# Kernel optimization log

Measured on AMD Instinct MI355X. Metric: run time of the kernel, lower is better.

The kernel has to match this reference:

```python
import jax, jax.numpy as jnp
import numpy as np

EPS = 1e-6
LOSS_WEIGHT = 1.0


def setup_inputs() -> dict:
    key = jax.random.key(0)
    k1, k2 = jax.random.split(key)
    pred = jax.random.normal(k1, (32, 2048, 2), dtype=jnp.float32)
    target = jax.random.normal(k2, (32, 2048, 2), dtype=jnp.float32)
    return {"pred": pred, "target": target}


def reference(pred, target):
    # Pairwise distances: [B, N1, N2]
    diff = pred[:, :, None, :] - target[:, None, :, :]
    sq = jnp.sum(diff * diff, axis=-1)
    dist = jnp.sqrt(sq + EPS)
    # Bidirectional Chamfer per batch item: [B]
    forward_chamfer = jnp.mean(jnp.min(dist, axis=2), axis=1)
    backward_chamfer = jnp.mean(jnp.min(dist, axis=1), axis=1)
    chamfer = forward_chamfer + backward_chamfer
    # reduction='mean' over batch -> scalar, scaled by loss_weight
    return LOSS_WEIGHT * jnp.mean(chamfer)
```

## Files before the change

kernel.cpp:

```cpp
#include <hip/hip_runtime.h>
#include <math.h>
#include <float.h>

#define B 32
#define N 2048
#define EPS 1e-6f
#define TILE 256
#define CHUNK 512
#define NCHUNK (N / CHUNK)
#define NTILES (N / TILE)
#define NQ_TOTAL (2 * B * N)

__global__ __launch_bounds__(256) void chamfer_min_kernel(
    const float* __restrict__ pred, const float* __restrict__ target,
    float* __restrict__ pmin) {
  const int tile = blockIdx.x;
  const int c    = blockIdx.y;
  const int db   = blockIdx.z;
  const int dir  = db >> 5;
  const int b    = db & 31;

  const float* qbase = (dir == 0) ? pred : target;
  const float* rbase = (dir == 0) ? target : pred;

  __shared__ float4 L[3 * CHUNK / 4];

  {
    const float4* rsrc = (const float4*)(rbase + (size_t)b * N * 2);
    float4 rv = rsrc[c * (CHUNK / 2) + threadIdx.x];
    float rx2a = -2.f * rv.x, ry2a = -2.f * rv.y;
    float rx2b = -2.f * rv.z, ry2b = -2.f * rv.w;
    float cra  = fmaf(rv.x, rv.x, rv.y * rv.y);
    float crb  = fmaf(rv.z, rv.z, rv.w * rv.w);
    float* Lf = (float*)L;
    const int base = 12 * (threadIdx.x >> 1) + 2 * (threadIdx.x & 1);
    *(float2*)(Lf + base + 0) = make_float2(rx2a, rx2b);
    *(float2*)(Lf + base + 4) = make_float2(ry2a, ry2b);
    *(float2*)(Lf + base + 8) = make_float2(cra,  crb);
  }
  __syncthreads();

  const int qi = tile * TILE + threadIdx.x;
  const float2 q = ((const float2*)(qbase + (size_t)b * N * 2))[qi];

  float m0 = FLT_MAX, m1 = FLT_MAX;
#pragma unroll 4
  for (int jj = 0; jj < CHUNK / 4; ++jj) {
    float4 X = L[3 * jj];
    float4 Y = L[3 * jj + 1];
    float4 C = L[3 * jj + 2];
    float d0 = fmaf(X.x, q.x, fmaf(Y.x, q.y, C.x));
    float d1 = fmaf(X.y, q.x, fmaf(Y.y, q.y, C.y));
    float d2 = fmaf(X.z, q.x, fmaf(Y.z, q.y, C.z));
    float d3 = fmaf(X.w, q.x, fmaf(Y.w, q.y, C.w));
    m0 = fminf(fminf(m0, d0), d1);
    m1 = fminf(fminf(m1, d2), d3);
  }
  const float qq = fmaf(q.x, q.x, q.y * q.y);
  pmin[((size_t)db * NCHUNK + c) * N + qi] = fminf(m0, m1) + qq;
}

__global__ __launch_bounds__(256) void chamfer_combine_kernel(
    const float* __restrict__ pmin, float* __restrict__ partial2) {
  const int g  = blockIdx.x * 256 + threadIdx.x;
  const int db = g >> 11;
  const int qi = g & 2047;
  const float* p = pmin + (size_t)db * NCHUNK * N + qi;
  float v = fminf(fminf(p[0], p[N]), fminf(p[2 * N], p[3 * N]));
  float s = sqrtf(fmaxf(v, 0.f) + EPS);
#pragma unroll
  for (int off = 32; off > 0; off >>= 1)
    s += __shfl_down(s, off, 64);
  __shared__ float wsum[4];
  const int wid = threadIdx.x >> 6;
  if ((threadIdx.x & 63) == 0) wsum[wid] = s;
  __syncthreads();
  if (threadIdx.x == 0)
    partial2[blockIdx.x] = wsum[0] + wsum[1] + wsum[2] + wsum[3];
}

__global__ __launch_bounds__(512) void chamfer_final_kernel(
    const float* __restrict__ partial2, float* __restrict__ out) {
  float v = partial2[threadIdx.x];
#pragma unroll
  for (int off = 32; off > 0; off >>= 1)
    v += __shfl_down(v, off, 64);
  __shared__ float wsum[8];
  if ((threadIdx.x & 63) == 0) wsum[threadIdx.x >> 6] = v;
  __syncthreads();
  if (threadIdx.x == 0) {
    float s = 0.f;
#pragma unroll
    for (int i = 0; i < 8; ++i) s += wsum[i];
    out[0] = s * (1.0f / (float)(B * N));
  }
}

extern "C" void kernel_launch(void* const* d_in, const int* in_sizes, int n_in,
                              void* d_out, int out_size, void* d_ws, size_t ws_size,
                              hipStream_t stream) {
  const float* pred   = (const float*)d_in[0];
  const float* target = (const float*)d_in[1];
  float* out = (float*)d_out;

  float* pmin     = (float*)d_ws;
  float* partial2 = (float*)d_ws + (size_t)2 * B * NCHUNK * N;

  dim3 grid1(NTILES, NCHUNK, 2 * B);
  chamfer_min_kernel<<<grid1, TILE, 0, stream>>>(pred, target, pmin);
  chamfer_combine_kernel<<<NQ_TOTAL / 256, 256, 0, stream>>>(pmin, partial2);
  chamfer_final_kernel<<<1, 512, 0, stream>>>(partial2, out);
}
```

Measured before the change: 31.91 us.

## Register-block eight queries per thread to reuse shared reference loads

The min kernel now keeps eight query points per thread in registers and streams smaller 128-point reference chunks from shared memory, so each LDS load feeds eight queries. The grid is reorganised into 16 chunks by query groups, and the partial-min buffer becomes chunk-major. The combine kernel reduces over 16 chunk partials instead of 4, which increases global traffic for the intermediate buffer.

New measurement: 29.23 us. -8.4%, faster.

```diff
diff --git a/kernel.cpp b/kernel.cpp
--- a/kernel.cpp
+++ b/kernel.cpp
@@ -5,75 +5,81 @@
 #define B 32
 #define N 2048
 #define EPS 1e-6f
-#define TILE 256
-#define CHUNK 512
-#define NCHUNK (N / CHUNK)
-#define NTILES (N / TILE)
+#define T1 128
+#define Q 8
+#define CHUNK 128
+#define C 16
 #define NQ_TOTAL (2 * B * N)
 
-__global__ __launch_bounds__(256) void chamfer_min_kernel(
+__global__ __launch_bounds__(128) void chamfer_minq8_kernel(
     const float* __restrict__ pred, const float* __restrict__ target,
     float* __restrict__ pmin) {
-  const int tile = blockIdx.x;
-  const int c    = blockIdx.y;
-  const int db   = blockIdx.z;
-  const int dir  = db >> 5;
-  const int b    = db & 31;
+  const int c  = blockIdx.x;
+  const int qg = blockIdx.y;
+  const int db = qg >> 1;
+  const int half = qg & 1;
+  const int dir = db >> 5;
+  const int b   = db & 31;
 
-  const float* qbase = (dir == 0) ? pred : target;
-  const float* rbase = (dir == 0) ? target : pred;
+  const float* qraw = (dir ? target : pred) + (size_t)b * N * 2;
+  const float* rraw = (dir ? pred : target) + (size_t)b * N * 2;
 
-  __shared__ float4 L[3 * CHUNK / 4];
+  __shared__ float Lf[3 * CHUNK];
 
   {
-    const float4* rsrc = (const float4*)(rbase + (size_t)b * N * 2);
-    float4 rv = rsrc[c * (CHUNK / 2) + threadIdx.x];
-    float rx2a = -2.f * rv.x, ry2a = -2.f * rv.y;
-    float rx2b = -2.f * rv.z, ry2b = -2.f * rv.w;
-    float cra  = fmaf(rv.x, rv.x, rv.y * rv.y);
-    float crb  = fmaf(rv.z, rv.z, rv.w * rv.w);
-    float* Lf = (float*)L;
-    const int base = 12 * (threadIdx.x >> 1) + 2 * (threadIdx.x & 1);
-    *(float2*)(Lf + base + 0) = make_float2(rx2a, rx2b);
-    *(float2*)(Lf + base + 4) = make_float2(ry2a, ry2b);
-    *(float2*)(Lf + base + 8) = make_float2(cra,  crb);
+    const float2 rv = ((const float2*)rraw)[c * CHUNK + threadIdx.x];
+    const int g = threadIdx.x >> 2, e = threadIdx.x & 3;
+    Lf[12 * g + e]     = -2.f * rv.x;
+    Lf[12 * g + 4 + e] = -2.f * rv.y;
+    Lf[12 * g + 8 + e] = fmaf(rv.x, rv.x, rv.y * rv.y);
   }
   __syncthreads();
 
-  const int qi = tile * TILE + threadIdx.x;
-  const float2 q = ((const float2*)(qbase + (size_t)b * N * 2))[qi];
+  float qx[Q], qy[Q], m[Q];
+#pragma unroll
+  for (int k = 0; k < Q; ++k) {
+    const float2 qp = ((const float2*)qraw)[half * 1024 + k * T1 + threadIdx.x];
+    qx[k] = qp.x;
+    qy[k] = qp.y;
+    m[k] = FLT_MAX;
+  }
 
-  float m0 = FLT_MAX, m1 = FLT_MAX;
 #pragma unroll 4
   for (int jj = 0; jj < CHUNK / 4; ++jj) {
-    float4 X = L[3 * jj];
-    float4 Y = L[3 * jj + 1];
-    float4 C = L[3 * jj + 2];
-    float d0 = fmaf(X.x, q.x, fmaf(Y.x, q.y, C.x));
-    float d1 = fmaf(X.y, q.x, fmaf(Y.y, q.y, C.y));
-    float d2 = fmaf(X.z, q.x, fmaf(Y.z, q.y, C.z));
-    float d3 = fmaf(X.w, q.x, fmaf(Y.w, q.y, C.w));
-    m0 = fminf(fminf(m0, d0), d1);
-    m1 = fminf(fminf(m1, d2), d3);
+    const float4 X = *(const float4*)(Lf + 12 * jj);
+    const float4 Y = *(const float4*)(Lf + 12 * jj + 4);
+    const float4 Cr = *(const float4*)(Lf + 12 * jj + 8);
+#pragma unroll
+    for (int k = 0; k < Q; ++k) {
+      float d0 = fmaf(X.x, qx[k], fmaf(Y.x, qy[k], Cr.x));
+      float d1 = fmaf(X.y, qx[k], fmaf(Y.y, qy[k], Cr.y));
+      float d2 = fmaf(X.z, qx[k], fmaf(Y.z, qy[k], Cr.z));
+      float d3 = fmaf(X.w, qx[k], fmaf(Y.w, qy[k], Cr.w));
+      m[k] = fminf(fminf(m[k], d0), d1);
+      m[k] = fminf(fminf(m[k], d2), d3);
+    }
   }
-  const float qq = fmaf(q.x, q.x, q.y * q.y);
-  pmin[((size_t)db * NCHUNK + c) * N + qi] = fminf(m0, m1) + qq;
+
+#pragma unroll
+  for (int k = 0; k < Q; ++k) {
+    const float qq = fmaf(qx[k], qx[k], qy[k] * qy[k]);
+    pmin[(size_t)c * NQ_TOTAL + qg * 1024 + k * T1 + threadIdx.x] = m[k] + qq;
+  }
 }
 
 __global__ __launch_bounds__(256) void chamfer_combine_kernel(
     const float* __restrict__ pmin, float* __restrict__ partial2) {
-  const int g  = blockIdx.x * 256 + threadIdx.x;
-  const int db = g >> 11;
-  const int qi = g & 2047;
-  const float* p = pmin + (size_t)db * NCHUNK * N + qi;
-  float v = fminf(fminf(p[0], p[N]), fminf(p[2 * N], p[3 * N]));
+  const int q = blockIdx.x * 256 + threadIdx.x;
+  float v = FLT_MAX;
+#pragma unroll
+  for (int c = 0; c < C; ++c)
+    v = fminf(v, pmin[(size_t)c * NQ_TOTAL + q]);
   float s = sqrtf(fmaxf(v, 0.f) + EPS);
 #pragma unroll
   for (int off = 32; off > 0; off >>= 1)
     s += __shfl_down(s, off, 64);
   __shared__ float wsum[4];
-  const int wid = threadIdx.x >> 6;
-  if ((threadIdx.x & 63) == 0) wsum[wid] = s;
+  if ((threadIdx.x & 63) == 0) wsum[threadIdx.x >> 6] = s;
   __syncthreads();
   if (threadIdx.x == 0)
     partial2[blockIdx.x] = wsum[0] + wsum[1] + wsum[2] + wsum[3];
@@ -104,10 +110,10 @@
   float* out = (float*)d_out;
 
   float* pmin     = (float*)d_ws;
-  float* partial2 = (float*)d_ws + (size_t)2 * B * NCHUNK * N;
+  float* partial2 = (float*)d_ws + (size_t)C * NQ_TOTAL;
 
-  dim3 grid1(NTILES, NCHUNK, 2 * B);
-  chamfer_min_kernel<<<grid1, TILE, 0, stream>>>(pred, target, pmin);
+  dim3 grid1(C, 2 * B * N / (T1 * Q));
+  chamfer_minq8_kernel<<<grid1, T1, 0, stream>>>(pred, target, pmin);
   chamfer_combine_kernel<<<NQ_TOTAL / 256, 256, 0, stream>>>(pmin, partial2);
   chamfer_final_kernel<<<1, 512, 0, stream>>>(partial2, out);
 }
```
